# Optimization experiments

Hardware: AMD Instinct MI355X
Metric: run time of the kernel (lower is better)

Reference implementation:

```python
import jax, jax.numpy as jnp
import numpy as np
from jax import lax

B, T, C = 4, 1024, 1024
H, HEAD = 16, 64            # n_head, head size (K == V == HEAD)
TM_DIM, TD_DIM = 32, 64     # TIME_MIX_EXTRA_DIM, W_MIX_EXTRA_DIM
N_LAYER, LAYER_ID = 24, 12
EPS = 1e-5
HEAD_DIV = 8.0              # head_size_divisor


def setup_inputs() -> dict:
    key = jax.random.key(0)
    ks = jax.random.split(key, 10)
    r1 = 1.0 - LAYER_ID / N_LAYER          # ratio_1_to_almost0
    r0 = LAYER_ID / max(N_LAYER - 1, 1)    # ratio_0_to_1
    ddd = np.arange(C, dtype=np.float64) / C
    x_maa = (1.0 - ddd ** r1).astype(np.float32)
    r_maa = (1.0 - ddd ** (0.5 * r1)).astype(np.float32)
    v_maa = (1.0 - (ddd ** r1 + 0.3 * r0)).astype(np.float32)
    n = np.arange(H * HEAD, dtype=np.float64)
    denom = max(H * HEAD - 1, 1)
    time_decay = (-6.0 + 5.0 * (n / denom) ** (0.7 + 1.3 * r0)).reshape(H, HEAD).astype(np.float32)
    zig = (((np.arange(H * HEAD) + 1) % 3) - 1) * 0.1
    time_first = (r0 * (1.0 - n / denom) + zig).reshape(H, HEAD).astype(np.float32)

    def unif(k, shape, s=0.01):
        return jax.random.uniform(k, shape, jnp.float32, -s, s)

    return {
        "x": jax.random.normal(ks[0], (B, T, C), jnp.float32),
        "x_maa": jnp.asarray(x_maa),
        "w_maa": jnp.asarray(x_maa),
        "k_maa": jnp.asarray(x_maa),
        "v_maa": jnp.asarray(v_maa),
        "r_maa": jnp.asarray(r_maa),
        "g_maa": jnp.asarray(r_maa),
        "tm_w1": unif(ks[1], (C, 5 * TM_DIM)),
        "tm_w2": unif(ks[2], (5, TM_DIM, C)),
        "td_w1": unif(ks[3], (C, TD_DIM)),
        "td_w2": unif(ks[4], (TD_DIM, C)),
        "time_decay": jnp.asarray(time_decay),
        "time_first": jnp.asarray(time_first),
        "Wr": jax.random.normal(ks[5], (C, H * HEAD), jnp.float32) * 0.02,
        "Wk": jax.random.normal(ks[6], (C, H * HEAD), jnp.float32) * 0.02,
        "Wv": jax.random.normal(ks[7], (C, H * HEAD), jnp.float32) * 0.02,
        "Wg": jax.random.normal(ks[8], (C, H * HEAD), jnp.float32) * 0.02,
        "Wo": jax.random.normal(ks[9], (H * HEAD, C), jnp.float32) * 0.02,
        "ln_w": jnp.ones((H * HEAD,), jnp.float32),
        "ln_b": jnp.zeros((H * HEAD,), jnp.float32),
    }


def reference(x, x_maa, w_maa, k_maa, v_maa, r_maa, g_maa,
              tm_w1, tm_w2, td_w1, td_w2, time_decay, time_first,
              Wr, Wk, Wv, Wg, Wo, ln_w, ln_b):
    B, T, C = x.shape
    H, K = time_decay.shape
    V = Wv.shape[1] // H
    # token shift: sx = x_{t-1} - x_t (zero-padded at t=0)
    sx = jnp.concatenate([jnp.zeros_like(x[:, :1]), x[:, :-1]], axis=1) - x
    # data-dependent token-mix LoRA: 5 mixing deltas
    mix = jnp.tanh((x + sx * x_maa) @ tm_w1).reshape(B, T, 5, TM_DIM)
    mix = jnp.einsum('btfd,fdc->fbtc', mix, tm_w2)  # [5,B,T,C]
    mw, mk, mv, mr, mg = mix
    wx = x + sx * (w_maa + mw)
    kx = x + sx * (k_maa + mk)
    vx = x + sx * (v_maa + mv)
    rx = x + sx * (r_maa + mr)
    gx = x + sx * (g_maa + mg)
    r = (rx @ Wr).reshape(B, T, H, K)
    k = (kx @ Wk).reshape(B, T, H, K)
    v = (vx @ Wv).reshape(B, T, H, V)
    g = jax.nn.silu(gx @ Wg)                         # [B,T,H*V]
    # data-dependent decay via LoRA, then double-exp squash into (0,1)
    w = time_decay[None, None] + (jnp.tanh(wx @ td_w1) @ td_w2).reshape(B, T, H, K)
    w = jnp.exp(-jnp.exp(w))                         # [B,T,H,K]
    u = time_first                                   # [H,K]

    def step(s, inp):
        rt, kt, vt, wt = inp                         # [B,H,K],[B,H,K],[B,H,V],[B,H,K]
        kv = kt[..., None] * vt[..., None, :]        # [B,H,K,V] outer product
        y = jnp.einsum('bhk,bhkv->bhv', rt, s + u[None, :, :, None] * kv)
        return wt[..., None] * s + kv, y

    s0 = jnp.zeros((B, H, K, V), x.dtype)
    xs = (jnp.moveaxis(r, 1, 0), jnp.moveaxis(k, 1, 0),
          jnp.moveaxis(v, 1, 0), jnp.moveaxis(w, 1, 0))
    _, ys = lax.scan(step, s0, xs)                   # ys: [T,B,H,V]
    out = jnp.moveaxis(ys, 0, 1).reshape(B, T, H, V) / HEAD_DIV
    # GroupNorm with n_kv_head groups over dim_v channels -> per-head norm
    mu = out.mean(-1, keepdims=True)
    var = out.var(-1, keepdims=True)
    out = ((out - mu) * lax.rsqrt(var + EPS)).reshape(B, T, H * V) * ln_w + ln_b
    return (out * g) @ Wo
```

## Files before the change

kernel.cpp:

```cpp
#include <hip/hip_runtime.h>
#include <hip/hip_bf16.h>
#include <math.h>
#include <stdint.h>

constexpr int Bn = 4, Tn = 1024, Cn = 1024, Hn = 16;
constexpr int BT = Bn * Tn;
constexpr long long BTC = (long long)BT * Cn;
constexpr int CL = 64;
constexpr int NC = Tn / CL;

typedef __bf16 bf16x8_t __attribute__((ext_vector_type(8)));
typedef float f32x4_t __attribute__((ext_vector_type(4)));
typedef unsigned short us8_t __attribute__((ext_vector_type(8)));

__device__ __forceinline__ unsigned short f2bf_bits(float v) {
    __hip_bfloat16 h = __float2bfloat16(v);
    return *reinterpret_cast<unsigned short*>(&h);
}
__device__ __forceinline__ float bfbits2f(unsigned short u) {
    unsigned int x = (unsigned int)u << 16;
    return __uint_as_float(x);
}

__device__ __forceinline__ void gload16(const void* g, void* l) {
    auto const* gp = reinterpret_cast<const unsigned int __attribute__((address_space(1)))*>(
        reinterpret_cast<uintptr_t>(g));
    auto* lp = reinterpret_cast<unsigned int __attribute__((address_space(3)))*>(
        reinterpret_cast<uintptr_t>(l));
    __builtin_amdgcn_global_load_lds(gp, lp, 16, 0, 0);
}

__global__ __launch_bounds__(256) void prep_mixin(const float* __restrict__ x,
                                                  const float* __restrict__ x_maa,
                                                  __hip_bfloat16* __restrict__ out) {
    long long q = (long long)blockIdx.x * 256 + threadIdx.x;
    if (q * 4 >= BTC) return;
    long long idx = q * 4;
    int c = (int)(idx & (Cn - 1));
    long long bt = idx >> 10;
    int t = (int)(bt & (Tn - 1));
    float4 xv = *reinterpret_cast<const float4*>(x + idx);
    float4 xp = (t > 0) ? *reinterpret_cast<const float4*>(x + idx - Cn)
                        : make_float4(0.f, 0.f, 0.f, 0.f);
    float4 ma = *reinterpret_cast<const float4*>(x_maa + c);
    ushort4 o;
    o.x = f2bf_bits(xv.x + (xp.x - xv.x) * ma.x);
    o.y = f2bf_bits(xv.y + (xp.y - xv.y) * ma.y);
    o.z = f2bf_bits(xv.z + (xp.z - xv.z) * ma.z);
    o.w = f2bf_bits(xv.w + (xp.w - xv.w) * ma.w);
    *reinterpret_cast<ushort4*>(out + idx) = o;
}

__global__ __launch_bounds__(256) void transp5(const float* __restrict__ W0,
                                               const float* __restrict__ W1,
                                               const float* __restrict__ W2,
                                               const float* __restrict__ W3,
                                               const float* __restrict__ W4,
                                               __hip_bfloat16* __restrict__ T0,
                                               __hip_bfloat16* __restrict__ T1,
                                               __hip_bfloat16* __restrict__ T2,
                                               __hip_bfloat16* __restrict__ T3,
                                               __hip_bfloat16* __restrict__ T4) {
    int z = blockIdx.z;
    const float* W = (z == 0) ? W0 : (z == 1) ? W1 : (z == 2) ? W2 : (z == 3) ? W3 : W4;
    __hip_bfloat16* Wt = (z == 0) ? T0 : (z == 1) ? T1 : (z == 2) ? T2 : (z == 3) ? T3 : T4;
    __shared__ float tile[32][33];
    int c0 = blockIdx.x * 32, r0 = blockIdx.y * 32;
    int tx = threadIdx.x & 31, ty = threadIdx.x >> 5;
    #pragma unroll
    for (int i = 0; i < 4; i++)
        tile[ty + 8 * i][tx] = W[(size_t)(r0 + ty + 8 * i) * Cn + c0 + tx];
    __syncthreads();
    #pragma unroll
    for (int i = 0; i < 4; i++)
        Wt[(size_t)(c0 + ty + 8 * i) * Cn + r0 + tx] = __float2bfloat16(tile[tx][ty + 8 * i]);
}

__global__ __launch_bounds__(256) void transp_bf16(const float* __restrict__ W,
                                                   __hip_bfloat16* __restrict__ Wt,
                                                   int R, int Cc) {
    __shared__ float tile[32][33];
    int c0 = blockIdx.x * 32, r0 = blockIdx.y * 32;
    int tx = threadIdx.x & 31, ty = threadIdx.x >> 5;
    #pragma unroll
    for (int i = 0; i < 4; i++)
        tile[ty + 8 * i][tx] = W[(size_t)(r0 + ty + 8 * i) * Cc + c0 + tx];
    __syncthreads();
    #pragma unroll
    for (int i = 0; i < 4; i++)
        Wt[(size_t)(c0 + ty + 8 * i) * R + r0 + tx] = __float2bfloat16(tile[tx][ty + 8 * i]);
}

template <int EPI>
__global__ __launch_bounds__(256) void gemm_f32(const float* __restrict__ A,
                                                const float* __restrict__ Bm,
                                                float* __restrict__ C,
                                                int M, int N, int K,
                                                const float* __restrict__ extra) {
    __shared__ float As[16][64];
    __shared__ float Bs[16][64];
    int tid = threadIdx.x;
    int m0 = blockIdx.y * 64, n0 = blockIdx.x * 64;
    int tx = tid & 15, ty = tid >> 4;
    int ar = tid >> 2, ac = (tid & 3) * 4;
    int br = tid >> 4, bc = (tid & 15) * 4;
    float acc[4][4] = {};

    for (int k0 = 0; k0 < K; k0 += 16) {
        const float* ap = A + (size_t)(m0 + ar) * K + k0 + ac;
        float4 av = *reinterpret_cast<const float4*>(ap);
        As[ac + 0][ar] = av.x; As[ac + 1][ar] = av.y;
        As[ac + 2][ar] = av.z; As[ac + 3][ar] = av.w;
        float4 bv = *reinterpret_cast<const float4*>(Bm + (size_t)(k0 + br) * N + n0 + bc);
        *reinterpret_cast<float4*>(&Bs[br][bc]) = bv;
        __syncthreads();
        #pragma unroll
        for (int kk = 0; kk < 16; kk++) {
            float4 a4 = *reinterpret_cast<const float4*>(&As[kk][ty * 4]);
            float4 b4 = *reinterpret_cast<const float4*>(&Bs[kk][tx * 4]);
            float aa[4] = {a4.x, a4.y, a4.z, a4.w};
            float bb[4] = {b4.x, b4.y, b4.z, b4.w};
            #pragma unroll
            for (int i = 0; i < 4; i++)
                #pragma unroll
                for (int j = 0; j < 4; j++)
                    acc[i][j] = fmaf(aa[i], bb[j], acc[i][j]);
        }
        __syncthreads();
    }

    #pragma unroll
    for (int i = 0; i < 4; i++) {
        int row = m0 + ty * 4 + i;
        #pragma unroll
        for (int j = 0; j < 4; j++) {
            int col = n0 + tx * 4 + j;
            float v = acc[i][j];
            if (EPI == 3) v = -expf(extra[col] + v);
            C[(size_t)row * N + col] = v;
        }
    }
}

template <int KS>
__global__ __launch_bounds__(256) void gemm_f32_splitk(const float* __restrict__ A,
                                                       const float* __restrict__ Bm,
                                                       float* __restrict__ part,
                                                       int M, int N, int K) {
    __shared__ float As[16][64];
    __shared__ float Bs[16][64];
    int tid = threadIdx.x;
    int kp = blockIdx.x;
    int m0 = blockIdx.y * 64;
    int kbeg = kp * (K / KS), kend = kbeg + K / KS;
    int tx = tid & 15, ty = tid >> 4;
    int ar = tid >> 2, ac = (tid & 3) * 4;
    int br = tid >> 4, bc = (tid & 15) * 4;
    float acc[4][4] = {};

    for (int k0 = kbeg; k0 < kend; k0 += 16) {
        float4 av = *reinterpret_cast<const float4*>(A + (size_t)(m0 + ar) * K + k0 + ac);
        As[ac + 0][ar] = av.x; As[ac + 1][ar] = av.y;
        As[ac + 2][ar] = av.z; As[ac + 3][ar] = av.w;
        *reinterpret_cast<float4*>(&Bs[br][bc]) =
            *reinterpret_cast<const float4*>(Bm + (size_t)(k0 + br) * N + bc);
        __syncthreads();
        #pragma unroll
        for (int kk = 0; kk < 16; kk++) {
            float4 a4 = *reinterpret_cast<const float4*>(&As[kk][ty * 4]);
            float4 b4 = *reinterpret_cast<const float4*>(&Bs[kk][tx * 4]);
            float aa[4] = {a4.x, a4.y, a4.z, a4.w};
            float bb[4] = {b4.x, b4.y, b4.z, b4.w};
            #pragma unroll
            for (int i = 0; i < 4; i++)
                #pragma unroll
                for (int j = 0; j < 4; j++)
                    acc[i][j] = fmaf(aa[i], bb[j], acc[i][j]);
        }
        __syncthreads();
    }
    #pragma unroll
    for (int i = 0; i < 4; i++) {
        int row = m0 + ty * 4 + i;
        #pragma unroll
        for (int j = 0; j < 4; j++)
            part[((size_t)kp * M + row) * N + tx * 4 + j] = acc[i][j];
    }
}

template <int KS>
__global__ __launch_bounds__(256) void splitk_reduce_tanh(const float* __restrict__ part,
                                                          float* __restrict__ outp,
                                                          int total, size_t stride) {
    int i = blockIdx.x * 256 + threadIdx.x;
    if (i >= total) return;
    float s = 0.f;
    #pragma unroll
    for (int kp = 0; kp < KS; kp++) s += part[kp * stride + i];
    outp[i] = tanhf(s);
}

template <int KS>
__global__ __launch_bounds__(256) void splitk_reduce_tanh_bf(const float* __restrict__ part,
                                                             __hip_bfloat16* __restrict__ outp,
                                                             int total, size_t stride) {
    int i = blockIdx.x * 256 + threadIdx.x;
    if (i >= total) return;
    float s = 0.f;
    #pragma unroll
    for (int kp = 0; kp < KS; kp++) s += part[kp * stride + i];
    outp[i] = __float2bfloat16(tanhf(s));
}

template <int KS>
__global__ __launch_bounds__(256) void gemm_mfma_sk(const __hip_bfloat16* __restrict__ A,
                                                    const __hip_bfloat16* __restrict__ Bt,
                                                    float* __restrict__ part,
                                                    int M, int N, int K) {
    __shared__ alignas(16) unsigned short As[64 * 64];
    __shared__ alignas(16) unsigned short Bs[128 * 64];
    int tid = threadIdx.x;
    int m0 = blockIdx.y * 64, n0 = blockIdx.x * 128;
    int kp = blockIdx.z;
    int kbeg = kp * (K / KS), kend = kbeg + K / KS;
    int wave = tid >> 6, lane = tid & 63;
    int wm = (wave & 1) * 32, wn = (wave >> 1) * 64;
    int l15 = lane & 15, l4 = lane >> 4;
    f32x4_t acc[2][4] = {};

    for (int k0 = kbeg; k0 < kend; k0 += 64) {
        #pragma unroll
        for (int p = 0; p < 2; p++) {
            int cch = tid + p * 256;
            int row = cch >> 3, slot = cch & 7;
            int s2 = slot ^ (row & 7);
            *reinterpret_cast<us8_t*>(&As[row * 64 + s2 * 8]) =
                *reinterpret_cast<const us8_t*>(&A[(size_t)(m0 + row) * K + k0 + slot * 8]);
        }
        #pragma unroll
        for (int p = 0; p < 4; p++) {
            int cch = tid + p * 256;
            int row = cch >> 3, slot = cch & 7;
            int s2 = slot ^ (row & 7);
            int rowg = n0 + row; if (rowg > N - 1) rowg = N - 1;
            *reinterpret_cast<us8_t*>(&Bs[row * 64 + s2 * 8]) =
                *reinterpret_cast<const us8_t*>(&Bt[(size_t)rowg * K + k0 + slot * 8]);
        }
        __syncthreads();
        #pragma unroll
        for (int kw = 0; kw < 2; kw++) {
            int slot = kw * 4 + l4;
            bf16x8_t af[2], bfr[4];
            #pragma unroll
            for (int f = 0; f < 2; f++) {
                int ar = wm + f * 16 + l15;
                af[f] = *reinterpret_cast<const bf16x8_t*>(&As[ar * 64 + (slot ^ (ar & 7)) * 8]);
            }
            #pragma unroll
            for (int f = 0; f < 4; f++) {
                int br = wn + f * 16 + l15;
                bfr[f] = *reinterpret_cast<const bf16x8_t*>(&Bs[br * 64 + (slot ^ (br & 7)) * 8]);
            }
            #pragma unroll
            for (int i = 0; i < 2; i++)
                #pragma unroll
                for (int j = 0; j < 4; j++)
                    acc[i][j] = __builtin_amdgcn_mfma_f32_16x16x32_bf16(af[i], bfr[j], acc[i][j], 0, 0, 0);
        }
        __syncthreads();
    }

    #pragma unroll
    for (int i = 0; i < 2; i++) {
        int rbase = m0 + wm + i * 16 + l4 * 4;
        #pragma unroll
        for (int j = 0; j < 4; j++) {
            int col = n0 + wn + j * 16 + l15;
            if (col < N) {
                #pragma unroll
                for (int q = 0; q < 4; q++)
                    part[((size_t)kp * M + rbase + q) * N + col] = acc[i][j][q];
            }
        }
    }
}

__global__ __launch_bounds__(256) void dmix_gemm(const __hip_bfloat16* __restrict__ A,
                                                 const __hip_bfloat16* __restrict__ W2T,
                                                 const float* __restrict__ x,
                                                 const float* __restrict__ wmaa,
                                                 const float* __restrict__ kmaa,
                                                 const float* __restrict__ vmaa,
                                                 const float* __restrict__ rmaa,
                                                 const float* __restrict__ gmaa,
                                                 float* __restrict__ wx,
                                                 __hip_bfloat16* __restrict__ kxb,
                                                 __hip_bfloat16* __restrict__ vxb,
                                                 __hip_bfloat16* __restrict__ rxb,
                                                 __hip_bfloat16* __restrict__ gxb) {
    __shared__ alignas(16) unsigned short As[64 * 32];
    __shared__ alignas(16) unsigned short Bs[128 * 32];
    int tid = threadIdx.x;
    int m0 = blockIdx.x * 64, n0 = blockIdx.y * 128;
    int f  = blockIdx.z;
    int wave = tid >> 6, lane = tid & 63;
    int wm = (wave & 1) * 32, wn = (wave >> 1) * 64;
    int l15 = lane & 15, l4 = lane >> 4;
    int lrow2 = lane >> 2, ls = lane & 3;
    f32x4_t acc[2][4] = {};

    {
        int row = wave * 16 + lrow2;
        int gs = ls ^ (row & 3);
        gload16(&A[(size_t)(m0 + row) * 160 + f * 32 + gs * 8], &As[(wave * 16) * 32]);
    }
    #pragma unroll
    for (int ci = 0; ci < 2; ci++) {
        int r0 = wave * 32 + ci * 16;
        int row = r0 + lrow2;
        int gs = ls ^ (row & 3);
        gload16(&W2T[(size_t)(n0 + row) * 160 + f * 32 + gs * 8], &Bs[r0 * 32]);
    }
    __syncthreads();
    bf16x8_t af[2], bfr[4];
    #pragma unroll
    for (int i = 0; i < 2; i++) {
        int ar = wm + i * 16 + l15;
        af[i] = *reinterpret_cast<const bf16x8_t*>(&As[ar * 32 + ((l4 ^ (ar & 3)) * 8)]);
    }
    #pragma unroll
    for (int j = 0; j < 4; j++) {
        int br = wn + j * 16 + l15;
        bfr[j] = *reinterpret_cast<const bf16x8_t*>(&Bs[br * 32 + ((l4 ^ (br & 3)) * 8)]);
    }
    #pragma unroll
    for (int i = 0; i < 2; i++)
        #pragma unroll
        for (int j = 0; j < 4; j++)
            acc[i][j] = __builtin_amdgcn_mfma_f32_16x16x32_bf16(af[i], bfr[j], acc[i][j], 0, 0, 0);

    const float* maa = (f == 0) ? wmaa : (f == 1) ? kmaa : (f == 2) ? vmaa
                     : (f == 3) ? rmaa : gmaa;
    __hip_bfloat16* dstb = (f == 1) ? kxb : (f == 2) ? vxb : (f == 3) ? rxb : gxb;
    #pragma unroll
    for (int i = 0; i < 2; i++) {
        int rbase = m0 + wm + i * 16 + l4 * 4;
        #pragma unroll
        for (int j = 0; j < 4; j++) {
            int col = n0 + wn + j * 16 + l15;
            float mv = maa[col];
            #pragma unroll
            for (int q = 0; q < 4; q++) {
                int row = rbase + q;
                int t = row & (Tn - 1);
                size_t o = (size_t)row * Cn + col;
                float xv = x[o];
                float xp = (t > 0) ? x[o - Cn] : 0.f;
                float val = xv + (xp - xv) * (mv + acc[i][j][q]);
                if (f == 0) wx[o] = val;
                else        dstb[o] = __float2bfloat16(val);
            }
        }
    }
}

__global__ __launch_bounds__(256) void gemm_qkvg(const __hip_bfloat16* __restrict__ A0,
                                                 const __hip_bfloat16* __restrict__ A1,
                                                 const __hip_bfloat16* __restrict__ A2,
                                                 const __hip_bfloat16* __restrict__ A3,
                                                 const __hip_bfloat16* __restrict__ B0,
                                                 const __hip_bfloat16* __restrict__ B1,
                                                 const __hip_bfloat16* __restrict__ B2,
                                                 const __hip_bfloat16* __restrict__ B3,
                                                 __hip_bfloat16* __restrict__ C0,
                                                 __hip_bfloat16* __restrict__ C1,
                                                 __hip_bfloat16* __restrict__ C2,
                                                 __hip_bfloat16* __restrict__ C3,
                                                 int M, int N, int K) {
    int g = blockIdx.z;
    const __hip_bfloat16* A  = (g == 0) ? A0 : (g == 1) ? A1 : (g == 2) ? A2 : A3;
    const __hip_bfloat16* Bt = (g == 0) ? B0 : (g == 1) ? B1 : (g == 2) ? B2 : B3;
    __hip_bfloat16* Co = (g == 0) ? C0 : (g == 1) ? C1 : (g == 2) ? C2 : C3;
    __shared__ alignas(16) unsigned short As[64 * 64];
    __shared__ alignas(16) unsigned short Bs[128 * 64];
    int tid = threadIdx.x;
    int m0 = blockIdx.x * 64, n0 = blockIdx.y * 128;
    int wave = tid >> 6, lane = tid & 63;
    int wm = (wave & 1) * 32, wn = (wave >> 1) * 64;
    int l15 = lane & 15, l4 = lane >> 4;
    int lrow = lane >> 3, ls2 = lane & 7;
    f32x4_t acc[2][4] = {};

    for (int k0 = 0; k0 < K; k0 += 64) {
        #pragma unroll
        for (int ci = 0; ci < 2; ci++) {
            int r0 = wave * 16 + ci * 8;
            int row = r0 + lrow;
            int gs = ls2 ^ (row & 7);
            gload16(&A[(size_t)(m0 + row) * K + k0 + gs * 8], &As[r0 * 64]);
        }
        #pragma unroll
        for (int ci = 0; ci < 4; ci++) {
            int r0 = wave * 32 + ci * 8;
            int row = r0 + lrow;
            int gs = ls2 ^ (row & 7);
            gload16(&Bt[(size_t)(n0 + row) * K + k0 + gs * 8], &Bs[r0 * 64]);
        }
        __syncthreads();
        #pragma unroll
        for (int kw = 0; kw < 2; kw++) {
            int slot = kw * 4 + l4;
            bf16x8_t af[2], bfr[4];
            #pragma unroll
            for (int f = 0; f < 2; f++) {
                int ar = wm + f * 16 + l15;
                af[f] = *reinterpret_cast<const bf16x8_t*>(&As[ar * 64 + (slot ^ (ar & 7)) * 8]);
            }
            #pragma unroll
            for (int f = 0; f < 4; f++) {
                int br = wn + f * 16 + l15;
                bfr[f] = *reinterpret_cast<const bf16x8_t*>(&Bs[br * 64 + (slot ^ (br & 7)) * 8]);
            }
            #pragma unroll
            for (int i = 0; i < 2; i++)
                #pragma unroll
                for (int j = 0; j < 4; j++)
                    acc[i][j] = __builtin_amdgcn_mfma_f32_16x16x32_bf16(af[i], bfr[j], acc[i][j], 0, 0, 0);
        }
        __syncthreads();
    }

    #pragma unroll
    for (int i = 0; i < 2; i++) {
        int rbase = m0 + wm + i * 16 + l4 * 4;
        #pragma unroll
        for (int j = 0; j < 4; j++) {
            int col = n0 + wn + j * 16 + l15;
            #pragma unroll
            for (int q = 0; q < 4; q++) {
                float v = acc[i][j][q];
                if (g == 3) v = v / (1.f + expf(-v));
                Co[(size_t)(rbase + q) * N + col] = __float2bfloat16(v);
            }
        }
    }
}

__global__ __launch_bounds__(256) void gemm_mfma_gl(const __hip_bfloat16* __restrict__ A,
                                                    const __hip_bfloat16* __restrict__ Bt,
                                                    float* __restrict__ Cout,
                                                    int M, int N, int K) {
    __shared__ alignas(16) unsigned short As[64 * 64];
    __shared__ alignas(16) unsigned short Bs[128 * 64];
    int tid = threadIdx.x;
    int m0 = blockIdx.x * 64, n0 = blockIdx.y * 128;
    int wave = tid >> 6, lane = tid & 63;
    int wm = (wave & 1) * 32, wn = (wave >> 1) * 64;
    int l15 = lane & 15, l4 = lane >> 4;
    int lrow = lane >> 3, ls2 = lane & 7;
    f32x4_t acc[2][4] = {};

    for (int k0 = 0; k0 < K; k0 += 64) {
        #pragma unroll
        for (int ci = 0; ci < 2; ci++) {
            int r0 = wave * 16 + ci * 8;
            int row = r0 + lrow;
            int gs = ls2 ^ (row & 7);
            gload16(&A[(size_t)(m0 + row) * K + k0 + gs * 8], &As[r0 * 64]);
        }
        #pragma unroll
        for (int ci = 0; ci < 4; ci++) {
            int r0 = wave * 32 + ci * 8;
            int row = r0 + lrow;
            int gs = ls2 ^ (row & 7);
            gload16(&Bt[(size_t)(n0 + row) * K + k0 + gs * 8], &Bs[r0 * 64]);
        }
        __syncthreads();
        #pragma unroll
        for (int kw = 0; kw < 2; kw++) {
            int slot = kw * 4 + l4;
            bf16x8_t af[2], bfr[4];
            #pragma unroll
            for (int f = 0; f < 2; f++) {
                int ar = wm + f * 16 + l15;
                af[f] = *reinterpret_cast<const bf16x8_t*>(&As[ar * 64 + (slot ^ (ar & 7)) * 8]);
            }
            #pragma unroll
            for (int f = 0; f < 4; f++) {
                int br = wn + f * 16 + l15;
                bfr[f] = *reinterpret_cast<const bf16x8_t*>(&Bs[br * 64 + (slot ^ (br & 7)) * 8]);
            }
            #pragma unroll
            for (int i = 0; i < 2; i++)
                #pragma unroll
                for (int j = 0; j < 4; j++)
                    acc[i][j] = __builtin_amdgcn_mfma_f32_16x16x32_bf16(af[i], bfr[j], acc[i][j], 0, 0, 0);
        }
        __syncthreads();
    }

    #pragma unroll
    for (int i = 0; i < 2; i++) {
        int rbase = m0 + wm + i * 16 + l4 * 4;
        #pragma unroll
        for (int j = 0; j < 4; j++) {
            int col = n0 + wn + j * 16 + l15;
            #pragma unroll
            for (int q = 0; q < 4; q++)
                Cout[(size_t)(rbase + q) * N + col] = acc[i][j][q];
        }
    }
}

__global__ __launch_bounds__(256) void chunk_summary(const __hip_bfloat16* __restrict__ kb,
                                                     const __hip_bfloat16* __restrict__ vb,
                                                     const float* __restrict__ lw,
                                                     float* __restrict__ Bc,
                                                     float* __restrict__ Wtot) {
    int bid = blockIdx.x;
    int c = bid & 15, h = (bid >> 4) & 15, b = bid >> 8;
    size_t gbase = ((size_t)(b * Tn + c * CL) * Hn + h) * 64;
    int tid = threadIdx.x;
    __shared__ float linc[64][68];
    __shared__ float wtp[4][64];
    __shared__ alignas(16) __hip_bfloat16 kdT[64][72];
    __shared__ alignas(16) __hip_bfloat16 vsT[64][72];
    int wave = tid >> 6, lane = tid & 63;
    {
        float acc = 0.f;
        #pragma unroll
        for (int i = 0; i < 16; i++) {
            int t = wave * 16 + i;
            acc += lw[gbase + (size_t)t * 1024 + lane];
            linc[t][lane] = acc;
        }
        wtp[wave][lane] = acc;
    }
    __syncthreads();
    {
        float off = 0.f;
        for (int g = 0; g < wave; g++) off += wtp[g][lane];
        #pragma unroll
        for (int i = 0; i < 16; i++) linc[wave * 16 + i][lane] += off;
    }
    __syncthreads();
    int t4 = tid >> 2, c0 = (tid & 3) * 16;
    #pragma unroll
    for (int i = 0; i < 4; i++) {
        int ch = c0 + i * 4;
        size_t ga = gbase + (size_t)t4 * 1024 + ch;
        ushort4 ku = *reinterpret_cast<const ushort4*>(kb + ga);
        ushort4 vu = *reinterpret_cast<const ushort4*>(vb + ga);
        float kk[4] = {bfbits2f(ku.x), bfbits2f(ku.y), bfbits2f(ku.z), bfbits2f(ku.w)};
        float vv[4] = {bfbits2f(vu.x), bfbits2f(vu.y), bfbits2f(vu.z), bfbits2f(vu.w)};
        #pragma unroll
        for (int j = 0; j < 4; j++) {
            float li = linc[t4][ch + j];
            float lend = linc[63][ch + j];
            kdT[ch + j][t4] = __float2bfloat16(kk[j] * expf(lend - li));
            vsT[ch + j][t4] = __float2bfloat16(vv[j]);
        }
    }
    if (tid < 64) Wtot[(size_t)bid * 64 + tid] = expf(linc[63][tid]);
    __syncthreads();
    int l15 = lane & 15, l4q = lane >> 4;
    #pragma unroll
    for (int nt = 0; nt < 4; nt++) {
        f32x4_t acc = {};
        #pragma unroll
        for (int kt = 0; kt < 2; kt++) {
            bf16x8_t a = *reinterpret_cast<const bf16x8_t*>(&kdT[wave * 16 + l15][kt * 32 + l4q * 8]);
            bf16x8_t bb = *reinterpret_cast<const bf16x8_t*>(&vsT[nt * 16 + l15][kt * 32 + l4q * 8]);
            acc = __builtin_amdgcn_mfma_f32_16x16x32_bf16(a, bb, acc, 0, 0, 0);
        }
        #pragma unroll
        for (int q = 0; q < 4; q++) {
            int krow = wave * 16 + l4q * 4 + q;
            Bc[(size_t)bid * 4096 + (size_t)krow * 64 + nt * 16 + l15] = acc[q];
        }
    }
}

__global__ __launch_bounds__(256) void chunk_scan(const float* __restrict__ Bc,
                                                  const float* __restrict__ Wtot,
                                                  float* __restrict__ SbufT) {
    int bid = blockIdx.x;
    int bh = bid >> 2, vg = bid & 3;
    int kk = threadIdx.x >> 2;
    int v = vg * 16 + (threadIdx.x & 3) * 4;
    float4 S = make_float4(0.f, 0.f, 0.f, 0.f);
    for (int c = 0; c < NC; c++) {
        size_t base = (size_t)(bh * NC + c) * 4096;
        SbufT[base + (size_t)(v + 0) * 64 + kk] = S.x;
        SbufT[base + (size_t)(v + 1) * 64 + kk] = S.y;
        SbufT[base + (size_t)(v + 2) * 64 + kk] = S.z;
        SbufT[base + (size_t)(v + 3) * 64 + kk] = S.w;
        float wt = Wtot[(size_t)(bh * NC + c) * 64 + kk];
        float4 b4 = *reinterpret_cast<const float4*>(Bc + base + (size_t)kk * 64 + v);
        S.x = fmaf(wt, S.x, b4.x);
        S.y = fmaf(wt, S.y, b4.y);
        S.z = fmaf(wt, S.z, b4.z);
        S.w = fmaf(wt, S.w, b4.w);
    }
}

__global__ __launch_bounds__(256) void chunk_out(const __hip_bfloat16* __restrict__ rb,
                                                 const __hip_bfloat16* __restrict__ kb,
                                                 const __hip_bfloat16* __restrict__ vb,
                                                 const float* __restrict__ lw,
                                                 const float* __restrict__ SbufT,
                                                 const float* __restrict__ tf,
                                                 const __hip_bfloat16* __restrict__ gb,
                                                 const float* __restrict__ lnw,
                                                 const float* __restrict__ lnb,
                                                 __hip_bfloat16* __restrict__ fin) {
    int bid = blockIdx.x;
    int c = bid & 15, h = (bid >> 4) & 15, b = bid >> 8;
    size_t gbase = ((size_t)(b * Tn + c * CL) * Hn + h) * 64;
    int tid = threadIdx.x;
    __shared__ alignas(16) __hip_bfloat16 qs[64][72];
    __shared__ alignas(16) __hip_bfloat16 ks[64][72];
    __shared__ alignas(16) __hip_bfloat16 vsT[64][72];
    __shared__ alignas(16) __hip_bfloat16 scT[64][72];
    __shared__ alignas(16) float uni[64 * 68];
    __shared__ float wtp[4][64];
    __shared__ float diag[64];
    float (*linc)[68] = reinterpret_cast<float(*)[68]>(uni);
    __hip_bfloat16 (*asb)[72] = reinterpret_cast<__hip_bfloat16(*)[72]>(uni);
    int wave = tid >> 6, lane = tid & 63;
    {
        float acc = 0.f;
        #pragma unroll
        for (int i = 0; i < 16; i++) {
            int t = wave * 16 + i;
            acc += lw[gbase + (size_t)t * 1024 + lane];
            linc[t][lane] = acc;
        }
        wtp[wave][lane] = acc;
    }
    __syncthreads();
    {
        float off = 0.f;
        for (int g = 0; g < wave; g++) off += wtp[g][lane];
        #pragma unroll
        for (int i = 0; i < 16; i++) linc[wave * 16 + i][lane] += off;
    }
    __syncthreads();
    int t4 = tid >> 2, c0 = (tid & 3) * 16;
    float dpart = 0.f;
    #pragma unroll
    for (int i = 0; i < 4; i++) {
        int ch = c0 + i * 4;
        size_t ga = gbase + (size_t)t4 * 1024 + ch;
        ushort4 ru = *reinterpret_cast<const ushort4*>(rb + ga);
        ushort4 ku = *reinterpret_cast<const ushort4*>(kb + ga);
        ushort4 vu = *reinterpret_cast<const ushort4*>(vb + ga);
        float4 l4v = *reinterpret_cast<const float4*>(lw + ga);
        float4 u4 = *reinterpret_cast<const float4*>(tf + h * 64 + ch);
        float4 s4 = *reinterpret_cast<const float4*>(SbufT + (size_t)bid * 4096 + (size_t)t4 * 64 + ch);
        float rr[4] = {bfbits2f(ru.x), bfbits2f(ru.y), bfbits2f(ru.z), bfbits2f(ru.w)};
        float kkv[4] = {bfbits2f(ku.x), bfbits2f(ku.y), bfbits2f(ku.z), bfbits2f(ku.w)};
        float vv[4] = {bfbits2f(vu.x), bfbits2f(vu.y), bfbits2f(vu.z), bfbits2f(vu.w)};
        float lwv[4] = {l4v.x, l4v.y, l4v.z, l4v.w};
        float uu[4] = {u4.x, u4.y, u4.z, u4.w};
        float ss[4] = {s4.x, s4.y, s4.z, s4.w};
        #pragma unroll
        for (int j = 0; j < 4; j++) {
            float li = linc[t4][ch + j];
            qs[t4][ch + j] = __float2bfloat16(rr[j] * expf(li - lwv[j]));
            ks[t4][ch + j] = __float2bfloat16(kkv[j] * expf(-li));
            vsT[ch + j][t4] = __float2bfloat16(vv[j]);
            scT[t4][ch + j] = __float2bfloat16(ss[j]);
            dpart = fmaf(rr[j] * uu[j], kkv[j], dpart);
        }
    }
    dpart += __shfl_xor(dpart, 1);
    dpart += __shfl_xor(dpart, 2);
    if ((tid & 3) == 0) diag[t4] = dpart;
    __syncthreads();
    int l15 = lane & 15, l4q = lane >> 4;
    #pragma unroll
    for (int nt = 0; nt < 4; nt++) {
        f32x4_t acc = {};
        if (nt <= wave) {
            #pragma unroll
            for (int kt = 0; kt < 2; kt++) {
                bf16x8_t a = *reinterpret_cast<const bf16x8_t*>(&qs[wave * 16 + l15][kt * 32 + l4q * 8]);
                bf16x8_t bb = *reinterpret_cast<const bf16x8_t*>(&ks[nt * 16 + l15][kt * 32 + l4q * 8]);
                acc = __builtin_amdgcn_mfma_f32_16x16x32_bf16(a, bb, acc, 0, 0, 0);
            }
        }
        #pragma unroll
        for (int q = 0; q < 4; q++) {
            int t = wave * 16 + l4q * 4 + q;
            int tau = nt * 16 + l15;
            float v = (tau < t) ? acc[q] : (tau == t ? diag[t] : 0.f);
            asb[t][tau] = __float2bfloat16(v);
        }
    }
    __syncthreads();
    f32x4_t oacc[4];
    #pragma unroll
    for (int nt = 0; nt < 4; nt++) {
        f32x4_t acc = {};
        int kmax = (wave >> 1) + 1;
        for (int kt = 0; kt < kmax; kt++) {
            bf16x8_t a = *reinterpret_cast<const bf16x8_t*>(&asb[wave * 16 + l15][kt * 32 + l4q * 8]);
            bf16x8_t bb = *reinterpret_cast<const bf16x8_t*>(&vsT[nt * 16 + l15][kt * 32 + l4q * 8]);
            acc = __builtin_amdgcn_mfma_f32_16x16x32_bf16(a, bb, acc, 0, 0, 0);
        }
        #pragma unroll
        for (int kt = 0; kt < 2; kt++) {
            bf16x8_t a = *reinterpret_cast<const bf16x8_t*>(&qs[wave * 16 + l15][kt * 32 + l4q * 8]);
            bf16x8_t bb = *reinterpret_cast<const bf16x8_t*>(&scT[nt * 16 + l15][kt * 32 + l4q * 8]);
            acc = __builtin_amdgcn_mfma_f32_16x16x32_bf16(a, bb, acc, 0, 0, 0);
        }
        oacc[nt] = acc;
    }
    float sum[4] = {0.f, 0.f, 0.f, 0.f}, sq[4] = {0.f, 0.f, 0.f, 0.f};
    #pragma unroll
    for (int nt = 0; nt < 4; nt++)
        #pragma unroll
        for (int q = 0; q < 4; q++) {
            float v = oacc[nt][q] * 0.125f;
            oacc[nt][q] = v;
            sum[q] += v;
            sq[q] += v * v;
        }
    #pragma unroll
    for (int off = 1; off < 16; off <<= 1)
        #pragma unroll
        for (int q = 0; q < 4; q++) {
            sum[q] += __shfl_xor(sum[q], off, 64);
            sq[q]  += __shfl_xor(sq[q],  off, 64);
        }
    float mu[4], rs[4];
    #pragma unroll
    for (int q = 0; q < 4; q++) {
        mu[q] = sum[q] * (1.f / 64.f);
        float var = sq[q] * (1.f / 64.f) - mu[q] * mu[q];
        rs[q] = rsqrtf(var + 1e-5f);
    }
    #pragma unroll
    for (int nt = 0; nt < 4; nt++) {
        int v = nt * 16 + l15;
        float lw_ = lnw[h * 64 + v];
        float lb_ = lnb[h * 64 + v];
        #pragma unroll
        for (int q = 0; q < 4; q++) {
            int t = wave * 16 + l4q * 4 + q;
            size_t o = gbase + (size_t)t * 1024 + v;
            float gv = bfbits2f(*reinterpret_cast<const unsigned short*>(&gb[o]));
            float val = (oacc[nt][q] - mu[q]) * rs[q] * lw_ + lb_;
            fin[o] = __float2bfloat16(val * gv);
        }
    }
}

extern "C" void kernel_launch(void* const* d_in, const int* in_sizes, int n_in,
                              void* d_out, int out_size, void* d_ws, size_t ws_size,
                              hipStream_t stream) {
    (void)in_sizes; (void)n_in; (void)out_size; (void)ws_size;
    const float* x      = (const float*)d_in[0];
    const float* x_maa  = (const float*)d_in[1];
    const float* w_maa  = (const float*)d_in[2];
    const float* k_maa  = (const float*)d_in[3];
    const float* v_maa  = (const float*)d_in[4];
    const float* r_maa  = (const float*)d_in[5];
    const float* g_maa  = (const float*)d_in[6];
    const float* tm_w1  = (const float*)d_in[7];
    const float* tm_w2  = (const float*)d_in[8];
    const float* td_w1  = (const float*)d_in[9];
    const float* td_w2  = (const float*)d_in[10];
    const float* t_dec  = (const float*)d_in[11];
    const float* t_first= (const float*)d_in[12];
    const float* Wr     = (const float*)d_in[13];
    const float* Wk     = (const float*)d_in[14];
    const float* Wv     = (const float*)d_in[15];
    const float* Wg     = (const float*)d_in[16];
    const float* Wo     = (const float*)d_in[17];
    const float* ln_w   = (const float*)d_in[18];
    const float* ln_b   = (const float*)d_in[19];
    float* out = (float*)d_out;

    char* ws = (char*)d_ws;
    size_t off = 0;
    auto alloc = [&](size_t bytes) -> void* {
        void* p = ws + off;
        off = (off + bytes + 255) & ~(size_t)255;
        return p;
    };
    __hip_bfloat16* mixin = (__hip_bfloat16*)alloc(BTC * 2);
    __hip_bfloat16* mix160b = (__hip_bfloat16*)alloc((size_t)BT * 160 * 2);
    float* wxr    = (float*)alloc(BTC * 4);
    __hip_bfloat16* kxb = (__hip_bfloat16*)alloc(BTC * 2);
    __hip_bfloat16* vxb = (__hip_bfloat16*)alloc(BTC * 2);
    __hip_bfloat16* rxb = (__hip_bfloat16*)alloc(BTC * 2);
    __hip_bfloat16* gxb = (__hip_bfloat16*)alloc(BTC * 2);
    __hip_bfloat16* kb  = (__hip_bfloat16*)alloc(BTC * 2);
    __hip_bfloat16* vb  = (__hip_bfloat16*)alloc(BTC * 2);
    __hip_bfloat16* gb  = (__hip_bfloat16*)alloc(BTC * 2);
    float* wl1 = (float*)alloc((size_t)BT * 64 * 4);
    float* lwb = (float*)alloc(BTC * 4);
    __hip_bfloat16* WrT = (__hip_bfloat16*)alloc((size_t)Cn * Cn * 2);
    __hip_bfloat16* WkT = (__hip_bfloat16*)alloc((size_t)Cn * Cn * 2);
    __hip_bfloat16* WvT = (__hip_bfloat16*)alloc((size_t)Cn * Cn * 2);
    __hip_bfloat16* WgT = (__hip_bfloat16*)alloc((size_t)Cn * Cn * 2);
    __hip_bfloat16* WoT = (__hip_bfloat16*)alloc((size_t)Cn * Cn * 2);
    __hip_bfloat16* tmw1T = (__hip_bfloat16*)alloc((size_t)160 * Cn * 2);
    __hip_bfloat16* w2T   = (__hip_bfloat16*)alloc((size_t)Cn * 160 * 2);
    char* big = (char*)alloc((size_t)4 * BT * 160 * 4);
    float* lorapart = (float*)big;
    float* skpart = (float*)big;
    __hip_bfloat16* rb = mixin;
    float* BcB   = wxr;
    float* WtB   = wl1;
    float* SbufT = (float*)rxb;
    __hip_bfloat16* fin = kxb;

    dim3 blk(256);
    transp5<<<dim3(32, 32, 5), blk, 0, stream>>>(Wr, Wk, Wv, Wg, Wo,
                                                 WrT, WkT, WvT, WgT, WoT);
    transp_bf16<<<dim3(5, 32), blk, 0, stream>>>(tm_w1, tmw1T, Cn, 160);
    transp_bf16<<<dim3(32, 5), blk, 0, stream>>>(tm_w2, w2T, 160, Cn);
    prep_mixin<<<dim3((unsigned)(BTC / 1024)), blk, 0, stream>>>(x, x_maa, mixin);
    gemm_mfma_sk<4><<<dim3(2, 64, 4), blk, 0, stream>>>(mixin, tmw1T, lorapart, BT, 160, Cn);
    splitk_reduce_tanh_bf<4><<<dim3((BT * 160 + 255) / 256), blk, 0, stream>>>(
        lorapart, mix160b, BT * 160, (size_t)BT * 160);
    dmix_gemm<<<dim3(64, 8, 5), blk, 0, stream>>>(mix160b, w2T, x,
                                                  w_maa, k_maa, v_maa, r_maa, g_maa,
                                                  wxr, kxb, vxb, rxb, gxb);
    gemm_qkvg<<<dim3(64, 8, 4), blk, 0, stream>>>(rxb, kxb, vxb, gxb,
                                                  WrT, WkT, WvT, WgT,
                                                  rb, kb, vb, gb, BT, Cn, Cn);
    gemm_f32_splitk<8><<<dim3(8, 64), blk, 0, stream>>>(wxr, td_w1, skpart, BT, 64, Cn);
    splitk_reduce_tanh<8><<<dim3(BT * 64 / 256), blk, 0, stream>>>(skpart, wl1, BT * 64,
                                                                   (size_t)BT * 64);
    gemm_f32<3><<<dim3(16, 64), blk, 0, stream>>>(wl1, td_w2, lwb, BT, Cn, 64, t_dec);
    chunk_summary<<<dim3(Bn * Hn * NC), blk, 0, stream>>>(kb, vb, lwb, BcB, WtB);
    chunk_scan<<<dim3(Bn * Hn * 4), blk, 0, stream>>>(BcB, WtB, SbufT);
    chunk_out<<<dim3(Bn * Hn * NC), blk, 0, stream>>>(rb, kb, vb, lwb, SbufT, t_first,
                                                      gb, ln_w, ln_b, fin);
    gemm_mfma_gl<<<dim3(64, 8), blk, 0, stream>>>(fin, WoT, out, BT, Cn, Cn);
}
```

Baseline: 197.1 us.

## Use 32x32 MFMA in QKVG GEMM and store chunk states in bf16

The fused r/k/v/g projection GEMM swaps its 16x16x32 MFMA tiles for 32x32x16 MFMA, so each wave issues fewer, larger matrix instructions and reads fewer LDS fragments per k-step. The chunk summary and prefix-state buffers (Bc, SbufT) now hold bf16 instead of fp32, which halves their memory traffic between the summary, scan and output kernels. The carried recurrence state is still accumulated in fp32, but per-chunk contributions and stored states lose precision.

```diff
diff --git a/kernel.cpp b/kernel.cpp
--- a/kernel.cpp
+++ b/kernel.cpp
@@ -11,6 +11,7 @@
 
 typedef __bf16 bf16x8_t __attribute__((ext_vector_type(8)));
 typedef float f32x4_t __attribute__((ext_vector_type(4)));
+typedef float f32x16_t __attribute__((ext_vector_type(16)));
 typedef unsigned short us8_t __attribute__((ext_vector_type(8)));
 
 __device__ __forceinline__ unsigned short f2bf_bits(float v) {
@@ -387,9 +388,9 @@
     int m0 = blockIdx.x * 64, n0 = blockIdx.y * 128;
     int wave = tid >> 6, lane = tid & 63;
     int wm = (wave & 1) * 32, wn = (wave >> 1) * 64;
-    int l15 = lane & 15, l4 = lane >> 4;
+    int l31 = lane & 31, l5 = lane >> 5;
     int lrow = lane >> 3, ls2 = lane & 7;
-    f32x4_t acc[2][4] = {};
+    f32x16_t acc[2] = {};
 
     for (int k0 = 0; k0 < K; k0 += 64) {
         #pragma unroll
@@ -408,40 +409,29 @@
         }
         __syncthreads();
         #pragma unroll
-        for (int kw = 0; kw < 2; kw++) {
-            int slot = kw * 4 + l4;
-            bf16x8_t af[2], bfr[4];
-            #pragma unroll
-            for (int f = 0; f < 2; f++) {
-                int ar = wm + f * 16 + l15;
-                af[f] = *reinterpret_cast<const bf16x8_t*>(&As[ar * 64 + (slot ^ (ar & 7)) * 8]);
+        for (int kt = 0; kt < 4; kt++) {
+            int slot = kt * 2 + l5;
+            int ar = wm + l31;
+            bf16x8_t a = *reinterpret_cast<const bf16x8_t*>(&As[ar * 64 + (slot ^ (ar & 7)) * 8]);
+            #pragma unroll
+            for (int j = 0; j < 2; j++) {
+                int br = wn + j * 32 + l31;
+                bf16x8_t b = *reinterpret_cast<const bf16x8_t*>(&Bs[br * 64 + (slot ^ (br & 7)) * 8]);
+                acc[j] = __builtin_amdgcn_mfma_f32_32x32x16_bf16(a, b, acc[j], 0, 0, 0);
             }
-            #pragma unroll
-            for (int f = 0; f < 4; f++) {
-                int br = wn + f * 16 + l15;
-                bfr[f] = *reinterpret_cast<const bf16x8_t*>(&Bs[br * 64 + (slot ^ (br & 7)) * 8]);
-            }
-            #pragma unroll
-            for (int i = 0; i < 2; i++)
-                #pragma unroll
-                for (int j = 0; j < 4; j++)
-                    acc[i][j] = __builtin_amdgcn_mfma_f32_16x16x32_bf16(af[i], bfr[j], acc[i][j], 0, 0, 0);
-        }
-        __syncthreads();
-    }
-
-    #pragma unroll
-    for (int i = 0; i < 2; i++) {
-        int rbase = m0 + wm + i * 16 + l4 * 4;
-        #pragma unroll
-        for (int j = 0; j < 4; j++) {
-            int col = n0 + wn + j * 16 + l15;
-            #pragma unroll
-            for (int q = 0; q < 4; q++) {
-                float v = acc[i][j][q];
-                if (g == 3) v = v / (1.f + expf(-v));
-                Co[(size_t)(rbase + q) * N + col] = __float2bfloat16(v);
-            }
+        }
+        __syncthreads();
+    }
+
+    #pragma unroll
+    for (int j = 0; j < 2; j++) {
+        int col = n0 + wn + j * 32 + l31;
+        #pragma unroll
+        for (int r = 0; r < 16; r++) {
+            int row = m0 + wm + (r & 3) + 8 * (r >> 2) + 4 * l5;
+            float v = acc[j][r];
+            if (g == 3) v = v / (1.f + expf(-v));
+            Co[(size_t)row * N + col] = __float2bfloat16(v);
         }
     }
 }
@@ -515,7 +505,7 @@
 __global__ __launch_bounds__(256) void chunk_summary(const __hip_bfloat16* __restrict__ kb,
                                                      const __hip_bfloat16* __restrict__ vb,
                                                      const float* __restrict__ lw,
-                                                     float* __restrict__ Bc,
+                                                     __hip_bfloat16* __restrict__ Bc,
                                                      float* __restrict__ Wtot) {
     int bid = blockIdx.x;
     int c = bid & 15, h = (bid >> 4) & 15, b = bid >> 8;
@@ -576,14 +566,14 @@
         #pragma unroll
         for (int q = 0; q < 4; q++) {
             int krow = wave * 16 + l4q * 4 + q;
-            Bc[(size_t)bid * 4096 + (size_t)krow * 64 + nt * 16 + l15] = acc[q];
-        }
-    }
-}
-
-__global__ __launch_bounds__(256) void chunk_scan(const float* __restrict__ Bc,
+            Bc[(size_t)bid * 4096 + (size_t)krow * 64 + nt * 16 + l15] = __float2bfloat16(acc[q]);
+        }
+    }
+}
+
+__global__ __launch_bounds__(256) void chunk_scan(const __hip_bfloat16* __restrict__ Bc,
                                                   const float* __restrict__ Wtot,
-                                                  float* __restrict__ SbufT) {
+                                                  __hip_bfloat16* __restrict__ SbufT) {
     int bid = blockIdx.x;
     int bh = bid >> 2, vg = bid & 3;
     int kk = threadIdx.x >> 2;
@@ -591,16 +581,16 @@
     float4 S = make_float4(0.f, 0.f, 0.f, 0.f);
     for (int c = 0; c < NC; c++) {
         size_t base = (size_t)(bh * NC + c) * 4096;
-        SbufT[base + (size_t)(v + 0) * 64 + kk] = S.x;
-        SbufT[base + (size_t)(v + 1) * 64 + kk] = S.y;
-        SbufT[base + (size_t)(v + 2) * 64 + kk] = S.z;
-        SbufT[base + (size_t)(v + 3) * 64 + kk] = S.w;
+        SbufT[base + (size_t)(v + 0) * 64 + kk] = __float2bfloat16(S.x);
+        SbufT[base + (size_t)(v + 1) * 64 + kk] = __float2bfloat16(S.y);
+        SbufT[base + (size_t)(v + 2) * 64 + kk] = __float2bfloat16(S.z);
+        SbufT[base + (size_t)(v + 3) * 64 + kk] = __float2bfloat16(S.w);
         float wt = Wtot[(size_t)(bh * NC + c) * 64 + kk];
-        float4 b4 = *reinterpret_cast<const float4*>(Bc + base + (size_t)kk * 64 + v);
-        S.x = fmaf(wt, S.x, b4.x);
-        S.y = fmaf(wt, S.y, b4.y);
-        S.z = fmaf(wt, S.z, b4.z);
-        S.w = fmaf(wt, S.w, b4.w);
+        ushort4 b4 = *reinterpret_cast<const ushort4*>(Bc + base + (size_t)kk * 64 + v);
+        S.x = fmaf(wt, S.x, bfbits2f(b4.x));
+        S.y = fmaf(wt, S.y, bfbits2f(b4.y));
+        S.z = fmaf(wt, S.z, bfbits2f(b4.z));
+        S.w = fmaf(wt, S.w, bfbits2f(b4.w));
     }
 }
 
@@ -608,7 +598,7 @@
                                                  const __hip_bfloat16* __restrict__ kb,
                                                  const __hip_bfloat16* __restrict__ vb,
                                                  const float* __restrict__ lw,
-                                                 const float* __restrict__ SbufT,
+                                                 const __hip_bfloat16* __restrict__ SbufT,
                                                  const float* __restrict__ tf,
                                                  const __hip_bfloat16* __restrict__ gb,
                                                  const float* __restrict__ lnw,
@@ -657,20 +647,20 @@
         ushort4 vu = *reinterpret_cast<const ushort4*>(vb + ga);
         float4 l4v = *reinterpret_cast<const float4*>(lw + ga);
         float4 u4 = *reinterpret_cast<const float4*>(tf + h * 64 + ch);
-        float4 s4 = *reinterpret_cast<const float4*>(SbufT + (size_t)bid * 4096 + (size_t)t4 * 64 + ch);
+        ushort4 s4 = *reinterpret_cast<const ushort4*>(SbufT + (size_t)bid * 4096 + (size_t)t4 * 64 + ch);
         float rr[4] = {bfbits2f(ru.x), bfbits2f(ru.y), bfbits2f(ru.z), bfbits2f(ru.w)};
         float kkv[4] = {bfbits2f(ku.x), bfbits2f(ku.y), bfbits2f(ku.z), bfbits2f(ku.w)};
         float vv[4] = {bfbits2f(vu.x), bfbits2f(vu.y), bfbits2f(vu.z), bfbits2f(vu.w)};
         float lwv[4] = {l4v.x, l4v.y, l4v.z, l4v.w};
         float uu[4] = {u4.x, u4.y, u4.z, u4.w};
-        float ss[4] = {s4.x, s4.y, s4.z, s4.w};
+        unsigned short ssb[4] = {s4.x, s4.y, s4.z, s4.w};
         #pragma unroll
         for (int j = 0; j < 4; j++) {
             float li = linc[t4][ch + j];
             qs[t4][ch + j] = __float2bfloat16(rr[j] * expf(li - lwv[j]));
             ks[t4][ch + j] = __float2bfloat16(kkv[j] * expf(-li));
             vsT[ch + j][t4] = __float2bfloat16(vv[j]);
-            scT[t4][ch + j] = __float2bfloat16(ss[j]);
+            *reinterpret_cast<unsigned short*>(&scT[t4][ch + j]) = ssb[j];
             dpart = fmaf(rr[j] * uu[j], kkv[j], dpart);
         }
     }
@@ -813,9 +803,9 @@
     float* lorapart = (float*)big;
     float* skpart = (float*)big;
     __hip_bfloat16* rb = mixin;
-    float* BcB   = wxr;
+    __hip_bfloat16* BcB = (__hip_bfloat16*)wxr;
     float* WtB   = wl1;
-    float* SbufT = (float*)rxb;
+    __hip_bfloat16* SbufT = rxb;
     __hip_bfloat16* fin = kxb;
 
     dim3 blk(256);
```

Result: no change. 196.5 us (-0.3%).

## Fuse token-shift mixing into LoRA GEMM, merge transposes, store chunk states in bf16

Applied to the files above, without the earlier changes.

Three changes. The separate prep_mixin kernel is removed, and the token-shift interpolation plus bf16 conversion now happen inside the A-tile load of the split-K LoRA GEMM. The three weight-transpose launches become one launch with a 7-slice grid, where the extra blocks of the two small slices return early. The chunk summary and the scan state buffers switch from fp32 to bf16, which halves their traffic and lets chunk_out copy the state bits without converting. The cost is that the GEMM now reads fp32 x (twice, for the previous row) once per N-tile block, and the recurrent state carries bf16 precision.

```diff
diff --git a/kernel.cpp b/kernel.cpp
--- a/kernel.cpp
+++ b/kernel.cpp
@@ -30,55 +30,35 @@
     __builtin_amdgcn_global_load_lds(gp, lp, 16, 0, 0);
 }
 
-__global__ __launch_bounds__(256) void prep_mixin(const float* __restrict__ x,
-                                                  const float* __restrict__ x_maa,
-                                                  __hip_bfloat16* __restrict__ out) {
-    long long q = (long long)blockIdx.x * 256 + threadIdx.x;
-    if (q * 4 >= BTC) return;
-    long long idx = q * 4;
-    int c = (int)(idx & (Cn - 1));
-    long long bt = idx >> 10;
-    int t = (int)(bt & (Tn - 1));
-    float4 xv = *reinterpret_cast<const float4*>(x + idx);
-    float4 xp = (t > 0) ? *reinterpret_cast<const float4*>(x + idx - Cn)
-                        : make_float4(0.f, 0.f, 0.f, 0.f);
-    float4 ma = *reinterpret_cast<const float4*>(x_maa + c);
-    ushort4 o;
-    o.x = f2bf_bits(xv.x + (xp.x - xv.x) * ma.x);
-    o.y = f2bf_bits(xv.y + (xp.y - xv.y) * ma.y);
-    o.z = f2bf_bits(xv.z + (xp.z - xv.z) * ma.z);
-    o.w = f2bf_bits(xv.w + (xp.w - xv.w) * ma.w);
-    *reinterpret_cast<ushort4*>(out + idx) = o;
-}
-
-__global__ __launch_bounds__(256) void transp5(const float* __restrict__ W0,
+__global__ __launch_bounds__(256) void transp7(const float* __restrict__ W0,
                                                const float* __restrict__ W1,
                                                const float* __restrict__ W2,
                                                const float* __restrict__ W3,
                                                const float* __restrict__ W4,
+                                               const float* __restrict__ W5,
+                                               const float* __restrict__ W6,
                                                __hip_bfloat16* __restrict__ T0,
                                                __hip_bfloat16* __restrict__ T1,
                                                __hip_bfloat16* __restrict__ T2,
                                                __hip_bfloat16* __restrict__ T3,
-                                               __hip_bfloat16* __restrict__ T4) {
+                                               __hip_bfloat16* __restrict__ T4,
+                                               __hip_bfloat16* __restrict__ T5,
+                                               __hip_bfloat16* __restrict__ T6) {
     int z = blockIdx.z;
-    const float* W = (z == 0) ? W0 : (z == 1) ? W1 : (z == 2) ? W2 : (z == 3) ? W3 : W4;
-    __hip_bfloat16* Wt = (z == 0) ? T0 : (z == 1) ? T1 : (z == 2) ? T2 : (z == 3) ? T3 : T4;
-    __shared__ float tile[32][33];
-    int c0 = blockIdx.x * 32, r0 = blockIdx.y * 32;
-    int tx = threadIdx.x & 31, ty = threadIdx.x >> 5;
-    #pragma unroll
-    for (int i = 0; i < 4; i++)
-        tile[ty + 8 * i][tx] = W[(size_t)(r0 + ty + 8 * i) * Cn + c0 + tx];
-    __syncthreads();
-    #pragma unroll
-    for (int i = 0; i < 4; i++)
-        Wt[(size_t)(c0 + ty + 8 * i) * Cn + r0 + tx] = __float2bfloat16(tile[tx][ty + 8 * i]);
-}
-
-__global__ __launch_bounds__(256) void transp_bf16(const float* __restrict__ W,
-                                                   __hip_bfloat16* __restrict__ Wt,
-                                                   int R, int Cc) {
+    const float* W;
+    __hip_bfloat16* Wt;
+    int R, Cc;
+    if (z < 5) {
+        W = (z == 0) ? W0 : (z == 1) ? W1 : (z == 2) ? W2 : (z == 3) ? W3 : W4;
+        Wt = (z == 0) ? T0 : (z == 1) ? T1 : (z == 2) ? T2 : (z == 3) ? T3 : T4;
+        R = Cn; Cc = Cn;
+    } else if (z == 5) {
+        if (blockIdx.x >= 5) return;
+        W = W5; Wt = T5; R = Cn; Cc = 160;
+    } else {
+        if (blockIdx.y >= 5) return;
+        W = W6; Wt = T6; R = 160; Cc = Cn;
+    }
     __shared__ float tile[32][33];
     int c0 = blockIdx.x * 32, r0 = blockIdx.y * 32;
     int tx = threadIdx.x & 31, ty = threadIdx.x >> 5;
@@ -213,7 +193,8 @@
 }
 
 template <int KS>
-__global__ __launch_bounds__(256) void gemm_mfma_sk(const __hip_bfloat16* __restrict__ A,
+__global__ __launch_bounds__(256) void gemm_mfma_sk(const float* __restrict__ x,
+                                                    const float* __restrict__ x_maa,
                                                     const __hip_bfloat16* __restrict__ Bt,
                                                     float* __restrict__ part,
                                                     int M, int N, int K) {
@@ -234,8 +215,29 @@
             int cch = tid + p * 256;
             int row = cch >> 3, slot = cch & 7;
             int s2 = slot ^ (row & 7);
-            *reinterpret_cast<us8_t*>(&As[row * 64 + s2 * 8]) =
-                *reinterpret_cast<const us8_t*>(&A[(size_t)(m0 + row) * K + k0 + slot * 8]);
+            int gr = m0 + row;
+            int t = gr & (Tn - 1);
+            size_t gx = (size_t)gr * Cn + k0 + slot * 8;
+            float4 xa0 = *reinterpret_cast<const float4*>(x + gx);
+            float4 xa1 = *reinterpret_cast<const float4*>(x + gx + 4);
+            float4 xp0 = make_float4(0.f, 0.f, 0.f, 0.f), xp1 = xp0;
+            if (t > 0) {
+                xp0 = *reinterpret_cast<const float4*>(x + gx - Cn);
+                xp1 = *reinterpret_cast<const float4*>(x + gx - Cn + 4);
+            }
+            float4 ma0 = *reinterpret_cast<const float4*>(x_maa + k0 + slot * 8);
+            float4 ma1 = *reinterpret_cast<const float4*>(x_maa + k0 + slot * 8 + 4);
+            ushort4 o0, o1;
+            o0.x = f2bf_bits(xa0.x + (xp0.x - xa0.x) * ma0.x);
+            o0.y = f2bf_bits(xa0.y + (xp0.y - xa0.y) * ma0.y);
+            o0.z = f2bf_bits(xa0.z + (xp0.z - xa0.z) * ma0.z);
+            o0.w = f2bf_bits(xa0.w + (xp0.w - xa0.w) * ma0.w);
+            o1.x = f2bf_bits(xa1.x + (xp1.x - xa1.x) * ma1.x);
+            o1.y = f2bf_bits(xa1.y + (xp1.y - xa1.y) * ma1.y);
+            o1.z = f2bf_bits(xa1.z + (xp1.z - xa1.z) * ma1.z);
+            o1.w = f2bf_bits(xa1.w + (xp1.w - xa1.w) * ma1.w);
+            *reinterpret_cast<ushort4*>(&As[row * 64 + s2 * 8]) = o0;
+            *reinterpret_cast<ushort4*>(&As[row * 64 + s2 * 8 + 4]) = o1;
         }
         #pragma unroll
         for (int p = 0; p < 4; p++) {
@@ -515,7 +517,7 @@
 __global__ __launch_bounds__(256) void chunk_summary(const __hip_bfloat16* __restrict__ kb,
                                                      const __hip_bfloat16* __restrict__ vb,
                                                      const float* __restrict__ lw,
-                                                     float* __restrict__ Bc,
+                                                     __hip_bfloat16* __restrict__ Bc,
                                                      float* __restrict__ Wtot) {
     int bid = blockIdx.x;
     int c = bid & 15, h = (bid >> 4) & 15, b = bid >> 8;
@@ -576,14 +578,14 @@
         #pragma unroll
         for (int q = 0; q < 4; q++) {
             int krow = wave * 16 + l4q * 4 + q;
-            Bc[(size_t)bid * 4096 + (size_t)krow * 64 + nt * 16 + l15] = acc[q];
-        }
-    }
-}
-
-__global__ __launch_bounds__(256) void chunk_scan(const float* __restrict__ Bc,
+            Bc[(size_t)bid * 4096 + (size_t)krow * 64 + nt * 16 + l15] = __float2bfloat16(acc[q]);
+        }
+    }
+}
+
+__global__ __launch_bounds__(256) void chunk_scan(const __hip_bfloat16* __restrict__ Bc,
                                                   const float* __restrict__ Wtot,
-                                                  float* __restrict__ SbufT) {
+                                                  __hip_bfloat16* __restrict__ SbufT) {
     int bid = blockIdx.x;
     int bh = bid >> 2, vg = bid & 3;
     int kk = threadIdx.x >> 2;
@@ -591,16 +593,16 @@
     float4 S = make_float4(0.f, 0.f, 0.f, 0.f);
     for (int c = 0; c < NC; c++) {
         size_t base = (size_t)(bh * NC + c) * 4096;
-        SbufT[base + (size_t)(v + 0) * 64 + kk] = S.x;
-        SbufT[base + (size_t)(v + 1) * 64 + kk] = S.y;
-        SbufT[base + (size_t)(v + 2) * 64 + kk] = S.z;
-        SbufT[base + (size_t)(v + 3) * 64 + kk] = S.w;
+        SbufT[base + (size_t)(v + 0) * 64 + kk] = __float2bfloat16(S.x);
+        SbufT[base + (size_t)(v + 1) * 64 + kk] = __float2bfloat16(S.y);
+        SbufT[base + (size_t)(v + 2) * 64 + kk] = __float2bfloat16(S.z);
+        SbufT[base + (size_t)(v + 3) * 64 + kk] = __float2bfloat16(S.w);
         float wt = Wtot[(size_t)(bh * NC + c) * 64 + kk];
-        float4 b4 = *reinterpret_cast<const float4*>(Bc + base + (size_t)kk * 64 + v);
-        S.x = fmaf(wt, S.x, b4.x);
-        S.y = fmaf(wt, S.y, b4.y);
-        S.z = fmaf(wt, S.z, b4.z);
-        S.w = fmaf(wt, S.w, b4.w);
+        ushort4 b4 = *reinterpret_cast<const ushort4*>(Bc + base + (size_t)kk * 64 + v);
+        S.x = fmaf(wt, S.x, bfbits2f(b4.x));
+        S.y = fmaf(wt, S.y, bfbits2f(b4.y));
+        S.z = fmaf(wt, S.z, bfbits2f(b4.z));
+        S.w = fmaf(wt, S.w, bfbits2f(b4.w));
     }
 }
 
@@ -608,7 +610,7 @@
                                                  const __hip_bfloat16* __restrict__ kb,
                                                  const __hip_bfloat16* __restrict__ vb,
                                                  const float* __restrict__ lw,
-                                                 const float* __restrict__ SbufT,
+                                                 const __hip_bfloat16* __restrict__ SbufT,
                                                  const float* __restrict__ tf,
                                                  const __hip_bfloat16* __restrict__ gb,
                                                  const float* __restrict__ lnw,
@@ -657,20 +659,20 @@
         ushort4 vu = *reinterpret_cast<const ushort4*>(vb + ga);
         float4 l4v = *reinterpret_cast<const float4*>(lw + ga);
         float4 u4 = *reinterpret_cast<const float4*>(tf + h * 64 + ch);
-        float4 s4 = *reinterpret_cast<const float4*>(SbufT + (size_t)bid * 4096 + (size_t)t4 * 64 + ch);
+        ushort4 s4 = *reinterpret_cast<const ushort4*>(SbufT + (size_t)bid * 4096 + (size_t)t4 * 64 + ch);
         float rr[4] = {bfbits2f(ru.x), bfbits2f(ru.y), bfbits2f(ru.z), bfbits2f(ru.w)};
         float kkv[4] = {bfbits2f(ku.x), bfbits2f(ku.y), bfbits2f(ku.z), bfbits2f(ku.w)};
         float vv[4] = {bfbits2f(vu.x), bfbits2f(vu.y), bfbits2f(vu.z), bfbits2f(vu.w)};
         float lwv[4] = {l4v.x, l4v.y, l4v.z, l4v.w};
         float uu[4] = {u4.x, u4.y, u4.z, u4.w};
-        float ss[4] = {s4.x, s4.y, s4.z, s4.w};
+        unsigned short ssb[4] = {s4.x, s4.y, s4.z, s4.w};
         #pragma unroll
         for (int j = 0; j < 4; j++) {
             float li = linc[t4][ch + j];
             qs[t4][ch + j] = __float2bfloat16(rr[j] * expf(li - lwv[j]));
             ks[t4][ch + j] = __float2bfloat16(kkv[j] * expf(-li));
             vsT[ch + j][t4] = __float2bfloat16(vv[j]);
-            scT[t4][ch + j] = __float2bfloat16(ss[j]);
+            *reinterpret_cast<unsigned short*>(&scT[t4][ch + j]) = ssb[j];
             dpart = fmaf(rr[j] * uu[j], kkv[j], dpart);
         }
     }
@@ -790,7 +792,7 @@
         off = (off + bytes + 255) & ~(size_t)255;
         return p;
     };
-    __hip_bfloat16* mixin = (__hip_bfloat16*)alloc(BTC * 2);
+    __hip_bfloat16* rb = (__hip_bfloat16*)alloc(BTC * 2);
     __hip_bfloat16* mix160b = (__hip_bfloat16*)alloc((size_t)BT * 160 * 2);
     float* wxr    = (float*)alloc(BTC * 4);
     __hip_bfloat16* kxb = (__hip_bfloat16*)alloc(BTC * 2);
@@ -812,19 +814,15 @@
     char* big = (char*)alloc((size_t)4 * BT * 160 * 4);
     float* lorapart = (float*)big;
     float* skpart = (float*)big;
-    __hip_bfloat16* rb = mixin;
-    float* BcB   = wxr;
+    __hip_bfloat16* BcB = (__hip_bfloat16*)wxr;
     float* WtB   = wl1;
-    float* SbufT = (float*)rxb;
+    __hip_bfloat16* SbufT = rxb;
     __hip_bfloat16* fin = kxb;
 
     dim3 blk(256);
-    transp5<<<dim3(32, 32, 5), blk, 0, stream>>>(Wr, Wk, Wv, Wg, Wo,
-                                                 WrT, WkT, WvT, WgT, WoT);
-    transp_bf16<<<dim3(5, 32), blk, 0, stream>>>(tm_w1, tmw1T, Cn, 160);
-    transp_bf16<<<dim3(32, 5), blk, 0, stream>>>(tm_w2, w2T, 160, Cn);
-    prep_mixin<<<dim3((unsigned)(BTC / 1024)), blk, 0, stream>>>(x, x_maa, mixin);
-    gemm_mfma_sk<4><<<dim3(2, 64, 4), blk, 0, stream>>>(mixin, tmw1T, lorapart, BT, 160, Cn);
+    transp7<<<dim3(32, 32, 7), blk, 0, stream>>>(Wr, Wk, Wv, Wg, Wo, tm_w1, tm_w2,
+                                                 WrT, WkT, WvT, WgT, WoT, tmw1T, w2T);
+    gemm_mfma_sk<4><<<dim3(2, 64, 4), blk, 0, stream>>>(x, x_maa, tmw1T, lorapart, BT, 160, Cn);
     splitk_reduce_tanh_bf<4><<<dim3((BT * 160 + 255) / 256), blk, 0, stream>>>(
         lorapart, mix160b, BT * 160, (size_t)BT * 160);
     dmix_gemm<<<dim3(64, 8, 5), blk, 0, stream>>>(mix160b, w2T, x,
```

Result: faster. 190.3 us (-3.5%).
